# Performance work log

Hardware: AMD Instinct MI355X
Metric: run time of the kernel (lower is better)

Reference implementation:

```python
import jax, jax.numpy as jnp
import numpy as np

H = 512   # hidden_size
L = 2     # decoder_layer
B = 64    # batch
T = 2048  # encoder sequence length


def setup_inputs() -> dict:
    key = jax.random.key(0)
    ks = jax.random.split(key, 9)
    hidden = jax.random.normal(ks[0], (L, B, H), dtype=jnp.float32)
    encoder_output = jax.random.normal(ks[1], (T, B, H), dtype=jnp.float32)
    enc_len = jax.random.randint(ks[2], (B,), T // 2, T + 1, dtype=jnp.int32)
    s = 0.02
    Wh = jax.random.normal(ks[3], (H, H), dtype=jnp.float32) * s  # hidden_proj
    bh = jnp.zeros((H,), dtype=jnp.float32)
    We = jax.random.normal(ks[4], (H, H), dtype=jnp.float32) * s  # encoder_output_proj
    be = jnp.zeros((H,), dtype=jnp.float32)
    Wo = jax.random.normal(ks[5], (H,), dtype=jnp.float32) * s    # out: Linear(H, 1)
    bo = jnp.zeros((1,), dtype=jnp.float32)
    return {"hidden": hidden, "encoder_output": encoder_output, "enc_len": enc_len,
            "Wh": Wh, "bh": bh, "We": We, "be": be, "Wo": Wo, "bo": bo}


def reference(hidden, encoder_output, enc_len, Wh, bh, We, be, Wo, bo):
    # encoder_output: [T,B,H] -> [B,T,H]
    enc = jnp.swapaxes(encoder_output, 0, 1)
    # bmm with (1/L) addMask == mean over decoder layers: [L,B,H] -> [B,H]
    h = jnp.mean(hidden, axis=0)
    hidden_attn = h @ Wh.T + bh                      # [B,H]
    enc_attn = jnp.einsum('bth,oh->bto', enc, We) + be  # [B,T,H]
    res = jnp.tanh(enc_attn + hidden_attn[:, None, :])  # [B,T,H]
    scores = res @ Wo + bo[0]                        # [B,T]
    # per-sample masked softmax over valid prefix [0:enc_len[i])
    mask = jnp.arange(T)[None, :] < enc_len[:, None]  # [B,T]
    neg = jnp.asarray(-jnp.inf, dtype=scores.dtype)
    w = jax.nn.softmax(jnp.where(mask, scores, neg), axis=1)
    w = jnp.where(mask, w, 0.0)
    return w[:, :, None]  # [B,T,1]
```

## Files before the change

kernel.cpp:

```cpp
#include <hip/hip_runtime.h>
#include <stdint.h>


typedef __attribute__((ext_vector_type(4))) float f32x4;
typedef __attribute__((ext_vector_type(8))) __bf16 bf16x8;
typedef __attribute__((ext_vector_type(8))) unsigned short u16x8;

#define AS3 __attribute__((address_space(3)))
#define AS1 __attribute__((address_space(1)))

__device__ __forceinline__ unsigned short f2bf(float f) {
  unsigned u = __builtin_bit_cast(unsigned, f);
  return (unsigned short)((u + 0x7FFFu + ((u >> 16) & 1u)) >> 16);
}

__device__ __forceinline__ float fast_tanh(float x) {
  float t = __expf(-2.0f * __builtin_fabsf(x));
  float r = (1.0f - t) * __builtin_amdgcn_rcpf(1.0f + t);
  return __builtin_copysignf(r, x);
}

__global__ void prep_comb_kernel(const float* __restrict__ hidden,
                                 const float* __restrict__ Wh,
                                 const float* __restrict__ bh,
                                 const float* __restrict__ be,
                                 float* __restrict__ comb) {
  __shared__ float hb[512];
  const int b = blockIdx.x, tid = threadIdx.x;
  for (int i = tid; i < 512; i += 256)
    hb[i] = 0.5f * (hidden[b * 512 + i] + hidden[32768 + b * 512 + i]);
  __syncthreads();
  for (int o = tid; o < 512; o += 256) {
    const f32x4* wr = (const f32x4*)(Wh + o * 512);
    const f32x4* hv = (const f32x4*)hb;
    float s = 0.f;
    for (int k = 0; k < 128; ++k) {
      f32x4 w = wr[k], x = hv[k];
      s += w.x * x.x + w.y * x.y + w.z * x.z + w.w * x.w;
    }
    comb[b * 512 + o] = s + bh[o] + be[o];
  }
}

__global__ void prep_pack_kernel(const float* __restrict__ We,
                                 unsigned short* __restrict__ wsw) {
  const int gid = blockIdx.x * 256 + threadIdx.x;
  const int s = gid >> 12;
  const int idx = gid & 4095;
  const int o = idx >> 3;
  const int sp = idx & 7;
  const int g = sp ^ (o & 7);
  const float* src = We + o * 512 + s * 64 + g * 8;
  u16x8 p;
#pragma unroll
  for (int e = 0; e < 8; ++e) p[e] = f2bf(src[e]);
  *(u16x8*)(wsw + (long)gid * 8) = p;
}

__global__ __launch_bounds__(512, 4) void gemm_score_kernel(
    const float* __restrict__ enc,
    const unsigned short* __restrict__ wsw,
    const float* __restrict__ comb,
    const float* __restrict__ Wo,
    float* __restrict__ scores)
{
  __shared__ __align__(16) unsigned char Blds[65536];
  __shared__ __align__(16) unsigned char Alds[64 * 144];
  __shared__ float spart[4][64];

  const int tid = threadIdx.x;
  const int lane = tid & 63;
  const int wave = tid >> 6;
  const int wm = wave >> 2;
  const int wn = wave & 3;
  const int l15 = lane & 15;
  const int lq = lane >> 4;

  const long r0 = (long)blockIdx.x * 64;

  const int arow = tid >> 3;
  const int ak8 = tid & 7;
  const float* aglb = enc + (r0 + arow) * 512 + ak8 * 8;
  unsigned char* awr = &Alds[arow * 144 + ak8 * 16];

  const unsigned char* bglb = (const unsigned char*)wsw + (long)tid * 16;

  const unsigned aoff0 = (unsigned)((wm * 32 + l15) * 144 + lq * 16);
  const int obase = wn * 128 + l15;
  const int o7 = l15 & 7;

  f32x4 acc[2][8];
#pragma unroll
  for (int i = 0; i < 2; ++i)
#pragma unroll
    for (int j = 0; j < 8; ++j) acc[i][j] = (f32x4){0.f, 0.f, 0.f, 0.f};

  f32x4 av0 = *(const f32x4*)(aglb);
  f32x4 av1 = *(const f32x4*)(aglb + 4);

  for (int ks = 0; ks < 8; ++ks) {
    const unsigned char* bs = bglb + (long)ks * 65536;
#pragma unroll
    for (int c = 0; c < 8; ++c) {
      __builtin_amdgcn_global_load_lds((const AS1 unsigned int*)(bs + c * 8192),
                                       (AS3 unsigned int*)(&Blds[tid * 16 + c * 8192]),
                                       16, 0, 0);
    }
    u16x8 p;
    p[0] = f2bf(av0.x); p[1] = f2bf(av0.y); p[2] = f2bf(av0.z); p[3] = f2bf(av0.w);
    p[4] = f2bf(av1.x); p[5] = f2bf(av1.y); p[6] = f2bf(av1.z); p[7] = f2bf(av1.w);
    *(u16x8*)awr = p;
    __syncthreads();

    if (ks < 7) {
      av0 = *(const f32x4*)(aglb + (ks + 1) * 64);
      av1 = *(const f32x4*)(aglb + (ks + 1) * 64 + 4);
    }

#pragma unroll
    for (int ksub = 0; ksub < 2; ++ksub) {
      bf16x8 af0 = *(const bf16x8*)(&Alds[aoff0 + ksub * 64]);
      bf16x8 af1 = *(const bf16x8*)(&Alds[aoff0 + 16 * 144 + ksub * 64]);
#pragma unroll
      for (int jn = 0; jn < 8; ++jn) {
        const int o = obase + jn * 16;
        const int g = ksub * 4 + lq;
        bf16x8 bf = *(const bf16x8*)(&Blds[o * 128 + ((g ^ o7) << 4)]);
        acc[0][jn] = __builtin_amdgcn_mfma_f32_16x16x32_bf16(af0, bf, acc[0][jn], 0, 0, 0);
        acc[1][jn] = __builtin_amdgcn_mfma_f32_16x16x32_bf16(af1, bf, acc[1][jn], 0, 0, 0);
      }
    }
    __syncthreads();
  }

  float ps[2][4];
#pragma unroll
  for (int i = 0; i < 2; ++i) {
#pragma unroll
    for (int q = 0; q < 4; ++q) {
      const int row = wm * 32 + i * 16 + lq * 4 + q;
      const float* crow = comb + row * 512;
      float s = 0.f;
#pragma unroll
      for (int jn = 0; jn < 8; ++jn) {
        const int col = obase + jn * 16;
        const float x = acc[i][jn][q] + crow[col];
        s += fast_tanh(x) * Wo[col];
      }
      ps[i][q] = s;
    }
  }
#pragma unroll
  for (int i = 0; i < 2; ++i)
#pragma unroll
    for (int q = 0; q < 4; ++q) {
      float s = ps[i][q];
      s += __shfl_xor(s, 1, 16);
      s += __shfl_xor(s, 2, 16);
      s += __shfl_xor(s, 4, 16);
      s += __shfl_xor(s, 8, 16);
      if (l15 == 0) spart[wn][wm * 32 + i * 16 + lq * 4 + q] = s;
    }
  __syncthreads();
  if (tid < 64) {
    float s = spart[0][tid] + spart[1][tid] + spart[2][tid] + spart[3][tid];
    scores[(long)tid * 2048 + blockIdx.x] = s;
  }
}

__global__ void softmax_kernel(const float* __restrict__ scores,
                               const int* __restrict__ enc_len,
                               float* __restrict__ out) {
  const int b = blockIdx.x;
  const int tid = threadIdx.x;
  const int lane = tid & 63;
  const int wv = tid >> 6;
  __shared__ float red[4];
  const int n = enc_len[b];
  const float* sc = scores + (long)b * 2048;

  float v[8];
  float m = -1e30f;
#pragma unroll
  for (int j = 0; j < 8; ++j) {
    const int t = tid + j * 256;
    v[j] = sc[t];
    if (t < n) m = fmaxf(m, v[j]);
  }
#pragma unroll
  for (int k = 32; k; k >>= 1) m = fmaxf(m, __shfl_xor(m, k, 64));
  if (lane == 0) red[wv] = m;
  __syncthreads();
  m = fmaxf(fmaxf(red[0], red[1]), fmaxf(red[2], red[3]));
  __syncthreads();

  float s = 0.f;
#pragma unroll
  for (int j = 0; j < 8; ++j) {
    const int t = tid + j * 256;
    const float e = (t < n) ? __expf(v[j] - m) : 0.f;
    v[j] = e;
    s += e;
  }
#pragma unroll
  for (int k = 32; k; k >>= 1) s += __shfl_xor(s, k, 64);
  if (lane == 0) red[wv] = s;
  __syncthreads();
  s = red[0] + red[1] + red[2] + red[3];
  const float inv = 1.0f / s;
#pragma unroll
  for (int j = 0; j < 8; ++j) {
    const int t = tid + j * 256;
    out[(long)b * 2048 + t] = v[j] * inv;
  }
}

extern "C" void kernel_launch(void* const* d_in, const int* in_sizes, int n_in,
                              void* d_out, int out_size, void* d_ws, size_t ws_size,
                              hipStream_t stream) {
  const float* hidden = (const float*)d_in[0];
  const float* enc    = (const float*)d_in[1];
  const int*   enclen = (const int*)d_in[2];
  const float* Wh     = (const float*)d_in[3];
  const float* bh     = (const float*)d_in[4];
  const float* We     = (const float*)d_in[5];
  const float* be     = (const float*)d_in[6];
  const float* Wo     = (const float*)d_in[7];
  float* out = (float*)d_out;

  uint8_t* ws = (uint8_t*)d_ws;
  unsigned short* wsw = (unsigned short*)ws;
  float* comb   = (float*)(ws + 524288);
  float* scores = (float*)(ws + 524288 + 131072);

  hipLaunchKernelGGL(prep_comb_kernel, dim3(64), dim3(256), 0, stream,
                     hidden, Wh, bh, be, comb);
  hipLaunchKernelGGL(prep_pack_kernel, dim3(128), dim3(256), 0, stream, We, wsw);
  hipLaunchKernelGGL(gemm_score_kernel, dim3(2048), dim3(512), 0, stream,
                     enc, wsw, comb, Wo, scores);
  hipLaunchKernelGGL(softmax_kernel, dim3(64), dim3(256), 0, stream,
                     scores, enclen, out);
}
```

Before: 164.3 us.

## Double-buffer GEMM LDS tiles with K=32 steps and new swizzle layout

```diff
diff --git a/kernel.cpp b/kernel.cpp
--- a/kernel.cpp
+++ b/kernel.cpp
@@ -5,6 +5,7 @@
 typedef __attribute__((ext_vector_type(4))) float f32x4;
 typedef __attribute__((ext_vector_type(8))) __bf16 bf16x8;
 typedef __attribute__((ext_vector_type(8))) unsigned short u16x8;
+typedef __attribute__((ext_vector_type(4))) unsigned short u16x4;
 
 #define AS3 __attribute__((address_space(3)))
 #define AS1 __attribute__((address_space(1)))
@@ -45,16 +46,16 @@
 __global__ void prep_pack_kernel(const float* __restrict__ We,
                                  unsigned short* __restrict__ wsw) {
   const int gid = blockIdx.x * 256 + threadIdx.x;
-  const int s = gid >> 12;
-  const int idx = gid & 4095;
-  const int o = idx >> 3;
-  const int sp = idx & 7;
-  const int g = sp ^ (o & 7);
-  const float* src = We + o * 512 + s * 64 + g * 8;
+  const int s = gid >> 11;
+  const int rem = gid & 2047;
+  const int o = rem >> 2;
+  const int g = rem & 3;
+  const float* src = We + o * 512 + s * 32 + g * 8;
   u16x8 p;
 #pragma unroll
   for (int e = 0; e < 8; ++e) p[e] = f2bf(src[e]);
-  *(u16x8*)(wsw + (long)gid * 8) = p;
+  const int dgran = s * 2048 + o * 4 + ((g ^ (o >> 1)) & 3);
+  *(u16x8*)(wsw + (long)dgran * 8) = p;
 }
 
 __global__ __launch_bounds__(512, 4) void gemm_score_kernel(
@@ -64,8 +65,8 @@
     const float* __restrict__ Wo,
     float* __restrict__ scores)
 {
-  __shared__ __align__(16) unsigned char Blds[65536];
-  __shared__ __align__(16) unsigned char Alds[64 * 144];
+  __shared__ __align__(16) unsigned char Blds[2][32768];
+  __shared__ __align__(16) unsigned char Alds[2][4096];
   __shared__ float spart[4][64];
 
   const int tid = threadIdx.x;
@@ -79,87 +80,96 @@
   const long r0 = (long)blockIdx.x * 64;
 
   const int arow = tid >> 3;
-  const int ak8 = tid & 7;
-  const float* aglb = enc + (r0 + arow) * 512 + ak8 * 8;
-  unsigned char* awr = &Alds[arow * 144 + ak8 * 16];
+  const int ac4 = tid & 7;
+  const float* aglb = enc + (r0 + arow) * 512 + ac4 * 4;
+  const unsigned awoff = (unsigned)(arow * 64 +
+                         ((((ac4 >> 1) ^ (arow >> 1)) & 3) << 4) + (ac4 & 1) * 8);
 
   const unsigned char* bglb = (const unsigned char*)wsw + (long)tid * 16;
 
-  const unsigned aoff0 = (unsigned)((wm * 32 + l15) * 144 + lq * 16);
-  const int obase = wn * 128 + l15;
-  const int o7 = l15 & 7;
+  const unsigned swz = (unsigned)(((lq ^ (l15 >> 1)) & 3) << 4);
+  const unsigned aoff = (unsigned)((wm * 32 + l15) * 64) + swz;
+  const unsigned boff = (unsigned)((wn * 128 + l15) * 64) + swz;
 
   f32x4 acc[2][8];
 #pragma unroll
-  for (int i = 0; i < 2; ++i)
-#pragma unroll
-    for (int j = 0; j < 8; ++j) acc[i][j] = (f32x4){0.f, 0.f, 0.f, 0.f};
-
-  f32x4 av0 = *(const f32x4*)(aglb);
-  f32x4 av1 = *(const f32x4*)(aglb + 4);
-
-  for (int ks = 0; ks < 8; ++ks) {
-    const unsigned char* bs = bglb + (long)ks * 65536;
-#pragma unroll
-    for (int c = 0; c < 8; ++c) {
-      __builtin_amdgcn_global_load_lds((const AS1 unsigned int*)(bs + c * 8192),
-                                       (AS3 unsigned int*)(&Blds[tid * 16 + c * 8192]),
-                                       16, 0, 0);
-    }
-    u16x8 p;
-    p[0] = f2bf(av0.x); p[1] = f2bf(av0.y); p[2] = f2bf(av0.z); p[3] = f2bf(av0.w);
-    p[4] = f2bf(av1.x); p[5] = f2bf(av1.y); p[6] = f2bf(av1.z); p[7] = f2bf(av1.w);
-    *(u16x8*)awr = p;
+  for (int m = 0; m < 2; ++m)
+#pragma unroll
+    for (int j = 0; j < 8; ++j) acc[m][j] = (f32x4){0.f, 0.f, 0.f, 0.f};
+
+  f32x4 av = *(const f32x4*)aglb;
+#pragma unroll
+  for (int c = 0; c < 4; ++c)
+    __builtin_amdgcn_global_load_lds((const AS1 unsigned int*)(bglb + c * 8192),
+                                     (AS3 unsigned int*)(&Blds[0][tid * 16 + c * 8192]),
+                                     16, 0, 0);
+  {
+    u16x4 p;
+    p[0] = f2bf(av.x); p[1] = f2bf(av.y); p[2] = f2bf(av.z); p[3] = f2bf(av.w);
+    *(u16x4*)(&Alds[0][awoff]) = p;
+  }
+  __syncthreads();
+
+  for (int ks = 0; ks < 16; ++ks) {
+    const int cur = ks & 1;
+    if (ks < 15) {
+      const unsigned char* bs = bglb + (long)(ks + 1) * 32768;
+#pragma unroll
+      for (int c = 0; c < 4; ++c)
+        __builtin_amdgcn_global_load_lds((const AS1 unsigned int*)(bs + c * 8192),
+                                         (AS3 unsigned int*)(&Blds[cur ^ 1][tid * 16 + c * 8192]),
+                                         16, 0, 0);
+      av = *(const f32x4*)(aglb + (ks + 1) * 32);
+    }
+
+    bf16x8 af0 = *(const bf16x8*)(&Alds[cur][aoff]);
+    bf16x8 af1 = *(const bf16x8*)(&Alds[cur][aoff + 1024]);
+#pragma unroll
+    for (int jn = 0; jn < 8; ++jn) {
+      bf16x8 bf = *(const bf16x8*)(&Blds[cur][boff + jn * 1024]);
+      acc[0][jn] = __builtin_amdgcn_mfma_f32_16x16x32_bf16(af0, bf, acc[0][jn], 0, 0, 0);
+      acc[1][jn] = __builtin_amdgcn_mfma_f32_16x16x32_bf16(af1, bf, acc[1][jn], 0, 0, 0);
+    }
+
+    if (ks < 15) {
+      u16x4 p;
+      p[0] = f2bf(av.x); p[1] = f2bf(av.y); p[2] = f2bf(av.z); p[3] = f2bf(av.w);
+      *(u16x4*)(&Alds[cur ^ 1][awoff]) = p;
+    }
     __syncthreads();
-
-    if (ks < 7) {
-      av0 = *(const f32x4*)(aglb + (ks + 1) * 64);
-      av1 = *(const f32x4*)(aglb + (ks + 1) * 64 + 4);
-    }
-
-#pragma unroll
-    for (int ksub = 0; ksub < 2; ++ksub) {
-      bf16x8 af0 = *(const bf16x8*)(&Alds[aoff0 + ksub * 64]);
-      bf16x8 af1 = *(const bf16x8*)(&Alds[aoff0 + 16 * 144 + ksub * 64]);
-#pragma unroll
-      for (int jn = 0; jn < 8; ++jn) {
-        const int o = obase + jn * 16;
-        const int g = ksub * 4 + lq;
-        bf16x8 bf = *(const bf16x8*)(&Blds[o * 128 + ((g ^ o7) << 4)]);
-        acc[0][jn] = __builtin_amdgcn_mfma_f32_16x16x32_bf16(af0, bf, acc[0][jn], 0, 0, 0);
-        acc[1][jn] = __builtin_amdgcn_mfma_f32_16x16x32_bf16(af1, bf, acc[1][jn], 0, 0, 0);
-      }
-    }
-    __syncthreads();
-  }
+  }
+
+  float wo[8];
+#pragma unroll
+  for (int jn = 0; jn < 8; ++jn) wo[jn] = Wo[wn * 128 + jn * 16 + l15];
 
   float ps[2][4];
 #pragma unroll
-  for (int i = 0; i < 2; ++i) {
+  for (int m = 0; m < 2; ++m) {
 #pragma unroll
     for (int q = 0; q < 4; ++q) {
-      const int row = wm * 32 + i * 16 + lq * 4 + q;
+      const int row = wm * 32 + m * 16 + lq * 4 + q;
       const float* crow = comb + row * 512;
       float s = 0.f;
 #pragma unroll
       for (int jn = 0; jn < 8; ++jn) {
-        const int col = obase + jn * 16;
-        const float x = acc[i][jn][q] + crow[col];
-        s += fast_tanh(x) * Wo[col];
+        const int col = wn * 128 + jn * 16 + l15;
+        const float x = acc[m][jn][q] + crow[col];
+        s += fast_tanh(x) * wo[jn];
       }
-      ps[i][q] = s;
-    }
-  }
-#pragma unroll
-  for (int i = 0; i < 2; ++i)
+      ps[m][q] = s;
+    }
+  }
+#pragma unroll
+  for (int m = 0; m < 2; ++m)
 #pragma unroll
     for (int q = 0; q < 4; ++q) {
-      float s = ps[i][q];
+      float s = ps[m][q];
       s += __shfl_xor(s, 1, 16);
       s += __shfl_xor(s, 2, 16);
       s += __shfl_xor(s, 4, 16);
       s += __shfl_xor(s, 8, 16);
-      if (l15 == 0) spart[wn][wm * 32 + i * 16 + lq * 4 + q] = s;
+      if (l15 == 0) spart[wn][wm * 32 + m * 16 + lq * 4 + q] = s;
     }
   __syncthreads();
   if (tid < 64) {
```

Result: slower. 184.5 us (+12.3%).
